# Kernel tuning notes

Hardware: AMD Instinct MI355X
Metric: run time of the kernel (lower is better)

Reference implementation:

```python
import jax, jax.numpy as jnp
import numpy as np


def setup_inputs() -> dict:
    key = jax.random.key(0)
    k1, k2, k3, k4 = jax.random.split(key, 4)
    B, T, C, D = 4, 2048, 1024, 128
    x = jax.random.normal(k1, (B, T, C), dtype=jnp.float32)
    # torch nn.Linear(in, out, bias=False) computes x @ W.T with W [out,in];
    # we store W as [in,out] so projection is x @ W (same math, transposed layout).
    Wq = jax.random.normal(k2, (C, D), dtype=jnp.float32) * (C ** -0.5)
    Wk = jax.random.normal(k3, (C, D), dtype=jnp.float32) * (C ** -0.5)
    Wv = jax.random.normal(k4, (C, D), dtype=jnp.float32) * (C ** -0.5)
    return {"x": x, "Wq": Wq, "Wk": Wk, "Wv": Wv}


def reference(x, Wq, Wk, Wv):
    B, T, C = x.shape
    D = Wq.shape[1]
    q = jnp.einsum("btc,cd->btd", x, Wq)
    k = jnp.einsum("btc,cd->btd", x, Wk)
    v = jnp.einsum("btc,cd->btd", x, Wv)
    scores = jnp.einsum("btd,bsd->bts", q, k) * (D ** -0.5)  # [B,T,T]
    causal = jnp.tril(jnp.ones((T, T), dtype=bool))
    scores = jnp.where(causal, scores, -jnp.inf)
    attn = jax.nn.softmax(scores, axis=-1)  # dropout_rate=0.0 -> identity
    return jnp.einsum("bts,bsd->btd", attn, v)
```

## Files before the change

kernel.cpp:

```cpp
#include <hip/hip_runtime.h>
#include <hip/hip_bf16.h>

typedef __attribute__((ext_vector_type(8))) short bf16x8;
typedef __attribute__((ext_vector_type(4))) short bf16x4;
typedef __attribute__((ext_vector_type(4))) float f32x4;

#define Tq 2048
#define Cq 1024
#define Dq 128

typedef const __attribute__((address_space(1))) void* gas_t;
typedef __attribute__((address_space(3))) void* las_t;

__device__ __forceinline__ short f2bf(float f) {
  unsigned u = __float_as_uint(f);
  u += 0x7fffu + ((u >> 16) & 1u);
  return (short)(u >> 16);
}

__global__ __launch_bounds__(256) void pack_w_kernel(const float* __restrict__ Wq_,
                                                     const float* __restrict__ Wk_,
                                                     const float* __restrict__ Wv_,
                                                     short* __restrict__ wt) {
  int tid = blockIdx.x * 256 + threadIdx.x;
  int y   = tid >> 14;
  int idx = tid & 16383;
  int kg  = idx >> 7;
  int n   = idx & 127;
  const float* W = (y == 0) ? Wq_ : (y == 1 ? Wk_ : Wv_);
  float scale = (y == 0) ? 0.08838834764831845f : 1.0f;
  bf16x8 o;
  #pragma unroll
  for (int j = 0; j < 8; ++j) o[j] = f2bf(W[(size_t)(kg * 8 + j) * Dq + n] * scale);
  *reinterpret_cast<bf16x8*>(wt + (size_t)y * 131072 + (size_t)n * 1024 + kg * 8) = o;
}

__global__ __launch_bounds__(128) void qkv_gemm_kernel(const float* __restrict__ x,
                                                       const short* __restrict__ wt,
                                                       short* __restrict__ qb,
                                                       short* __restrict__ kb2,
                                                       short* __restrict__ vt) {
  __shared__ float As[2][32][64];
  __shared__ short Bs[2][128][64];
  int y  = blockIdx.y;
  int bm = blockIdx.x;
  int w  = threadIdx.x >> 6, l = threadIdx.x & 63;
  int r  = l & 15, h = l >> 4;
  const short* wy = wt + (size_t)y * 131072;

  auto stage = [&](int t, int bi) {
    int k0 = t * 64;
    #pragma unroll
    for (int i = 0; i < 4; ++i) {
      int ia  = w * 4 + i;
      int row = ia * 4 + (l >> 4);
      int g   = l & 15;
      int sg  = (g & 8) | ((g & 7) ^ (row & 7));
      __builtin_amdgcn_global_load_lds(
          (gas_t)(x + (size_t)(bm * 32 + row) * Cq + k0 + sg * 4),
          (las_t)(&As[bi][ia * 4][0]), 16, 0, 0);
    }
    #pragma unroll
    for (int i = 0; i < 8; ++i) {
      int ib  = w * 8 + i;
      int row = ib * 8 + (l >> 3);
      int sc  = ((l & 7) ^ (row & 7)) * 8;
      __builtin_amdgcn_global_load_lds(
          (gas_t)(wy + (size_t)row * Cq + k0 + sc),
          (las_t)(&Bs[bi][ib * 8][0]), 16, 0, 0);
    }
  };

  f32x4 acc[2][4] = {};
  stage(0, 0);
  int cur = 0;
  for (int t = 0; t < 16; ++t, cur ^= 1) {
    stage(t + 1 < 16 ? t + 1 : t, cur ^ 1);
    asm volatile("s_waitcnt vmcnt(12)" ::: "memory");
    __builtin_amdgcn_s_barrier();
    __builtin_amdgcn_sched_barrier(0);
    bf16x8 af[2][2], bf[4][2];
    #pragma unroll
    for (int mi = 0; mi < 2; ++mi)
      #pragma unroll
      for (int kt = 0; kt < 2; ++kt) {
        int row = mi * 16 + r;
        int g0  = kt * 8 + h * 2;
        int s0  = (g0 & 8) | ((g0 & 7) ^ (row & 7));
        int g1  = g0 + 1;
        int s1  = (g1 & 8) | ((g1 & 7) ^ (row & 7));
        f32x4 fa = *reinterpret_cast<const f32x4*>(&As[cur][row][s0 * 4]);
        f32x4 fb = *reinterpret_cast<const f32x4*>(&As[cur][row][s1 * 4]);
        union { bf16x8 v; unsigned u[4]; } cv;
        asm("v_cvt_pk_bf16_f32 %0, %1, %2" : "=v"(cv.u[0]) : "v"(fa[0]), "v"(fa[1]));
        asm("v_cvt_pk_bf16_f32 %0, %1, %2" : "=v"(cv.u[1]) : "v"(fa[2]), "v"(fa[3]));
        asm("v_cvt_pk_bf16_f32 %0, %1, %2" : "=v"(cv.u[2]) : "v"(fb[0]), "v"(fb[1]));
        asm("v_cvt_pk_bf16_f32 %0, %1, %2" : "=v"(cv.u[3]) : "v"(fb[2]), "v"(fb[3]));
        af[mi][kt] = cv.v;
      }
    #pragma unroll
    for (int ni = 0; ni < 4; ++ni)
      #pragma unroll
      for (int kt = 0; kt < 2; ++kt) {
        int row = w * 64 + ni * 16 + r;
        bf[ni][kt] = *reinterpret_cast<const bf16x8*>(
            &Bs[cur][row][(kt * 32 + h * 8) ^ ((row & 7) << 3)]);
      }
    #pragma unroll
    for (int kt = 0; kt < 2; ++kt)
      #pragma unroll
      for (int mi = 0; mi < 2; ++mi)
        #pragma unroll
        for (int ni = 0; ni < 4; ++ni)
          acc[mi][ni] = __builtin_amdgcn_mfma_f32_16x16x32_bf16(af[mi][kt], bf[ni][kt], acc[mi][ni], 0, 0, 0);
    __builtin_amdgcn_sched_barrier(0);
    __builtin_amdgcn_s_barrier();
  }

  #pragma unroll
  for (int mi = 0; mi < 2; ++mi) {
    #pragma unroll
    for (int ni = 0; ni < 4; ++ni) {
      #pragma unroll
      for (int reg = 0; reg < 4; ++reg) {
        int m = bm * 32 + mi * 16 + h * 4 + reg;
        int n = w * 64 + ni * 16 + r;
        short s = f2bf(acc[mi][ni][reg]);
        if (y == 0)      qb[(size_t)m * Dq + n] = s;
        else if (y == 1) kb2[(size_t)m * Dq + n] = s;
        else {
          int bb = m >> 11, t2 = m & 2047;
          vt[((size_t)bb * Dq + n) * Tq + t2] = s;
        }
      }
    }
  }
}

__global__ __launch_bounds__(256, 4) void attn_kernel(const short* __restrict__ qb,
                                                      const short* __restrict__ kb2,
                                                      const short* __restrict__ vtb,
                                                      float* __restrict__ pacc,
                                                      float* __restrict__ pml) {
  __shared__ struct {
    short kb[2][32][128];
    short vb[2][128][32];
    short pb[4][16][40];
  } sm;

  int bid = blockIdx.x;
  int qi  = 31 - (bid >> 5);
  int b   = (bid >> 3) & 3;
  int c   = bid & 7;
  int tid = threadIdx.x;
  int w   = tid >> 6, l = tid & 63;
  int r   = l & 15, h = l >> 4;

  int qw = qi * 64 + w * 16;
  const short* kbB = kb2 + (size_t)b * Tq * Dq;
  const short* vtB = vtb + (size_t)b * Dq * Tq;

  bf16x8 aq[4];
  size_t qbase = ((size_t)b * Tq + qw + r) * Dq;
  #pragma unroll
  for (int kt = 0; kt < 4; ++kt)
    aq[kt] = *reinterpret_cast<const bf16x8*>(qb + qbase + kt * 32 + h * 8);

  int ntall = 2 * qi + 2;
  int clen  = (ntall + 7) >> 3;
  int tbeg  = c * clen;
  int tend  = ntall < tbeg + clen ? ntall : tbeg + clen;

  f32x4 acc[8] = {};
  float mrun = -1e30f, lrun = 0.0f;

  if (tbeg < tend) {
    auto stage = [&](int it, int bi) {
      int kv0 = it * 32;
      #pragma unroll
      for (int i2 = 0; i2 < 2; ++i2) {
        int i = w * 2 + i2;
        int row = i * 4 + (l >> 4);
        int sc  = ((l & 15) * 8) ^ ((row & 7) << 3);
        __builtin_amdgcn_global_load_lds(
            (gas_t)(kbB + (size_t)(kv0 + row) * Dq + sc),
            (las_t)(&sm.kb[bi][i * 4][0]), 16, 0, 0);
      }
      #pragma unroll
      for (int i2 = 0; i2 < 2; ++i2) {
        int i = w * 2 + i2;
        int row = i * 16 + (l >> 2);
        int sc  = ((l & 3) * 8) ^ ((row & 3) << 3);
        __builtin_amdgcn_global_load_lds(
            (gas_t)(vtB + (size_t)row * Tq + kv0 + sc),
            (las_t)(&sm.vb[bi][i * 16][0]), 16, 0, 0);
      }
    };

    stage(tbeg, 0);
    int cur = 0;
    for (int t = tbeg; t < tend; ++t, cur ^= 1) {
      stage(t + 1 < tend ? t + 1 : t, cur ^ 1);
      asm volatile("s_waitcnt vmcnt(4)" ::: "memory");
      __builtin_amdgcn_s_barrier();
      __builtin_amdgcn_sched_barrier(0);

      int kv0 = t * 32;
      bf16x8 kf[8];
      #pragma unroll
      for (int nt = 0; nt < 2; ++nt)
        #pragma unroll
        for (int kt = 0; kt < 4; ++kt) {
          int row = nt * 16 + r;
          kf[nt * 4 + kt] = *reinterpret_cast<const bf16x8*>(
              &sm.kb[cur][row][(kt * 32 + h * 8) ^ ((row & 7) << 3)]);
        }
      f32x4 s[2] = {};
      #pragma unroll
      for (int nt = 0; nt < 2; ++nt)
        #pragma unroll
        for (int kt = 0; kt < 4; ++kt)
          s[nt] = __builtin_amdgcn_mfma_f32_16x16x32_bf16(
              kf[nt * 4 + kt], aq[kt], s[nt], 0, 0, 0);

      bf16x8 vf[8];
      #pragma unroll
      for (int dt = 0; dt < 8; ++dt) {
        int row = dt * 16 + r;
        vf[dt] = *reinterpret_cast<const bf16x8*>(
            &sm.vb[cur][row][(h * 8) ^ ((row & 3) << 3)]);
      }

      if (kv0 + 31 > qw) {
        #pragma unroll
        for (int nt = 0; nt < 2; ++nt)
          #pragma unroll
          for (int reg = 0; reg < 4; ++reg)
            if (kv0 + nt * 16 + h * 4 + reg > qw + r) s[nt][reg] = -1e30f;
      }

      float mx = fmaxf(fmaxf(fmaxf(s[0][0], s[0][1]), fmaxf(s[0][2], s[0][3])),
                       fmaxf(fmaxf(s[1][0], s[1][1]), fmaxf(s[1][2], s[1][3])));
      mx = fmaxf(mx, __shfl_xor(mx, 16));
      mx = fmaxf(mx, __shfl_xor(mx, 32));
      float mnew  = fmaxf(mrun, mx);
      float alpha = __expf(mrun - mnew);
      mrun = mnew;
      float p[2][4];
      #pragma unroll
      for (int nt = 0; nt < 2; ++nt)
        #pragma unroll
        for (int reg = 0; reg < 4; ++reg)
          p[nt][reg] = s[nt][reg] > -1e29f ? __expf(s[nt][reg] - mnew) : 0.0f;
      float rsum = ((p[0][0] + p[0][1]) + (p[0][2] + p[0][3])) +
                   ((p[1][0] + p[1][1]) + (p[1][2] + p[1][3]));
      rsum += __shfl_xor(rsum, 16);
      rsum += __shfl_xor(rsum, 32);
      lrun = lrun * alpha + rsum;

      float af[4];
      #pragma unroll
      for (int reg = 0; reg < 4; ++reg) af[reg] = __shfl(alpha, h * 4 + reg);
      #pragma unroll
      for (int dt = 0; dt < 8; ++dt)
        #pragma unroll
        for (int reg = 0; reg < 4; ++reg) acc[dt][reg] *= af[reg];

      #pragma unroll
      for (int nt = 0; nt < 2; ++nt) {
        bf16x4 w4;
        #pragma unroll
        for (int reg = 0; reg < 4; ++reg) w4[reg] = f2bf(p[nt][reg]);
        *reinterpret_cast<bf16x4*>(&sm.pb[w][r][nt * 16 + h * 4]) = w4;
      }
      asm volatile("s_waitcnt lgkmcnt(0)" ::: "memory");
      __builtin_amdgcn_sched_barrier(0);
      bf16x8 ap = *reinterpret_cast<const bf16x8*>(&sm.pb[w][r][h * 8]);

      #pragma unroll
      for (int dt = 0; dt < 8; ++dt)
        acc[dt] = __builtin_amdgcn_mfma_f32_16x16x32_bf16(ap, vf[dt], acc[dt], 0, 0, 0);

      __builtin_amdgcn_sched_barrier(0);
      __builtin_amdgcn_s_barrier();
    }
  }

  if (h == 0) {
    pml[((size_t)bid * 64 + w * 16 + r) * 2 + 0] = mrun;
    pml[((size_t)bid * 64 + w * 16 + r) * 2 + 1] = lrun;
  }
  #pragma unroll
  for (int dt = 0; dt < 8; ++dt)
    #pragma unroll
    for (int reg = 0; reg < 4; ++reg) {
      int row = w * 16 + h * 4 + reg;
      pacc[((size_t)bid * 64 + row) * 128 + dt * 16 + r] = acc[dt][reg];
    }
}

__global__ __launch_bounds__(256) void combine_kernel(const float* __restrict__ pacc,
                                                      const float* __restrict__ pml,
                                                      float* __restrict__ out) {
  int gid = blockIdx.x * 256 + threadIdx.x;
  int rg  = gid >> 5;
  int c4  = (gid & 31) * 4;
  int task = rg >> 6;
  int row  = rg & 63;
  int qi = 31 - (task >> 2);
  int b  = task & 3;
  int bbase = task * 8;
  float M[8], L[8];
  float Ms = -1e30f;
  #pragma unroll
  for (int cc = 0; cc < 8; ++cc) {
    M[cc] = pml[((size_t)(bbase + cc) * 64 + row) * 2 + 0];
    L[cc] = pml[((size_t)(bbase + cc) * 64 + row) * 2 + 1];
    Ms = fmaxf(Ms, M[cc]);
  }
  float den = 0.0f;
  f32x4 num = {};
  #pragma unroll
  for (int cc = 0; cc < 8; ++cc) {
    float e = __expf(M[cc] - Ms);
    den += e * L[cc];
    f32x4 a = *reinterpret_cast<const f32x4*>(
        pacc + ((size_t)(bbase + cc) * 64 + row) * 128 + c4);
    num += a * e;
  }
  f32x4 o = num * (1.0f / den);
  *reinterpret_cast<f32x4*>(out + ((size_t)b * Tq + qi * 64 + row) * Dq + c4) = o;
}

extern "C" void kernel_launch(void* const* d_in, const int* in_sizes, int n_in,
                              void* d_out, int out_size, void* d_ws, size_t ws_size,
                              hipStream_t stream) {
  const float* x   = (const float*)d_in[0];
  const float* Wq_ = (const float*)d_in[1];
  const float* Wk_ = (const float*)d_in[2];
  const float* Wv_ = (const float*)d_in[3];
  float* out = (float*)d_out;
  char* ws = (char*)d_ws;
  short* wt   = (short*)(ws);
  short* qb   = (short*)(ws + 786432);
  short* kb   = (short*)(ws + 2883584);
  short* vt   = (short*)(ws + 4980736);
  float* pml  = (float*)(ws + 7077888);
  float* pacc = (float*)(ws + 7602176);

  hipLaunchKernelGGL(pack_w_kernel, dim3(192), dim3(256), 0, stream, Wq_, Wk_, Wv_, wt);
  hipLaunchKernelGGL(qkv_gemm_kernel, dim3(256, 3), dim3(128), 0, stream, x, wt, qb, kb, vt);
  hipLaunchKernelGGL(attn_kernel, dim3(1024), dim3(256), 0, stream, qb, kb, vt, pacc, pml);
  hipLaunchKernelGGL(combine_kernel, dim3(1024), dim3(256), 0, stream, pacc, pml, out);
}
```

Baseline: 56.63 us.

## Split causal attention into fixed-size KV chunks with variable chunk count per query tile

Replaces the fixed 8-way split of each query tile's KV range with fixed chunks of 4 KV tiles, so the number of blocks per query tile grows with its causal length (272 blocks per batch, 1088 total). This evens out per-block work and removes empty blocks from short query tiles. The combine kernel now reads a variable number of partials per row through closed-form offsets, and the workspace layout is shifted to hold the larger partial buffers. The costs are a serial loop to decode block indices, more partial results to write and merge, and fewer KV tiles per block, so each block does less pipelined work to hide its latency.

```diff
diff --git a/kernel.cpp b/kernel.cpp
--- a/kernel.cpp
+++ b/kernel.cpp
@@ -149,9 +149,11 @@
   } sm;
 
   int bid = blockIdx.x;
-  int qi  = 31 - (bid >> 5);
-  int b   = (bid >> 3) & 3;
-  int c   = bid & 7;
+  int b   = bid / 272;
+  int s0i = bid - b * 272;
+  int qi  = 31, off = 0;
+  while (s0i >= off + ((qi >> 1) + 1)) { off += (qi >> 1) + 1; --qi; }
+  int c   = s0i - off;
   int tid = threadIdx.x;
   int w   = tid >> 6, l = tid & 63;
   int r   = l & 15, h = l >> 4;
@@ -167,14 +169,13 @@
     aq[kt] = *reinterpret_cast<const bf16x8*>(qb + qbase + kt * 32 + h * 8);
 
   int ntall = 2 * qi + 2;
-  int clen  = (ntall + 7) >> 3;
-  int tbeg  = c * clen;
-  int tend  = ntall < tbeg + clen ? ntall : tbeg + clen;
+  int tbeg  = c * 4;
+  int tend  = ntall < tbeg + 4 ? ntall : tbeg + 4;
 
   f32x4 acc[8] = {};
   float mrun = -1e30f, lrun = 0.0f;
 
-  if (tbeg < tend) {
+  {
     auto stage = [&](int it, int bi) {
       int kv0 = it * 32;
       #pragma unroll
@@ -305,27 +306,27 @@
   int gid = blockIdx.x * 256 + threadIdx.x;
   int rg  = gid >> 5;
   int c4  = (gid & 31) * 4;
-  int task = rg >> 6;
-  int row  = rg & 63;
-  int qi = 31 - (task >> 2);
-  int b  = task & 3;
-  int bbase = task * 8;
-  float M[8], L[8];
+  int b      = rg >> 11;
+  int rowInB = rg & 2047;
+  int qi     = rowInB >> 6;
+  int row    = rowInB & 63;
+  int m    = qi >> 1;
+  int F    = (qi & 1) ? (m + 1) * (m + 2) : (m + 1) * (m + 1);
+  int base = b * 272 + 272 - F;
+  int nch  = m + 1;
+
   float Ms = -1e30f;
-  #pragma unroll
-  for (int cc = 0; cc < 8; ++cc) {
-    M[cc] = pml[((size_t)(bbase + cc) * 64 + row) * 2 + 0];
-    L[cc] = pml[((size_t)(bbase + cc) * 64 + row) * 2 + 1];
-    Ms = fmaxf(Ms, M[cc]);
-  }
+  for (int cc = 0; cc < nch; ++cc)
+    Ms = fmaxf(Ms, pml[((size_t)(base + cc) * 64 + row) * 2 + 0]);
   float den = 0.0f;
   f32x4 num = {};
-  #pragma unroll
-  for (int cc = 0; cc < 8; ++cc) {
-    float e = __expf(M[cc] - Ms);
-    den += e * L[cc];
+  for (int cc = 0; cc < nch; ++cc) {
+    float M = pml[((size_t)(base + cc) * 64 + row) * 2 + 0];
+    float L = pml[((size_t)(base + cc) * 64 + row) * 2 + 1];
+    float e = __expf(M - Ms);
+    den += e * L;
     f32x4 a = *reinterpret_cast<const f32x4*>(
-        pacc + ((size_t)(bbase + cc) * 64 + row) * 128 + c4);
+        pacc + ((size_t)(base + cc) * 64 + row) * 128 + c4);
     num += a * e;
   }
   f32x4 o = num * (1.0f / den);
@@ -346,10 +347,10 @@
   short* kb   = (short*)(ws + 2883584);
   short* vt   = (short*)(ws + 4980736);
   float* pml  = (float*)(ws + 7077888);
-  float* pacc = (float*)(ws + 7602176);
+  float* pacc = (float*)(ws + 7634944);
 
   hipLaunchKernelGGL(pack_w_kernel, dim3(192), dim3(256), 0, stream, Wq_, Wk_, Wv_, wt);
   hipLaunchKernelGGL(qkv_gemm_kernel, dim3(256, 3), dim3(128), 0, stream, x, wt, qb, kb, vt);
-  hipLaunchKernelGGL(attn_kernel, dim3(1024), dim3(256), 0, stream, qb, kb, vt, pacc, pml);
+  hipLaunchKernelGGL(attn_kernel, dim3(1088), dim3(256), 0, stream, qb, kb, vt, pacc, pml);
   hipLaunchKernelGGL(combine_kernel, dim3(1024), dim3(256), 0, stream, pacc, pml, out);
 }
```

Result: slower. 61.35 us (+8.3%).

## Keep P in registers via bpermute and store split-K partials as bf16

Applied to the files above, without the earlier changes.

Drops the LDS round-trip for the softmax probabilities. P is now packed to bf16 with v_cvt_pk_bf16_f32 and redistributed across lanes with ds_bpermute, and the PV MFMA operands are swapped so alpha rescaling needs no per-register shuffle. Partial accumulators written to the workspace and read by the combine kernel are now bf16 instead of fp32, which halves that traffic. The changes add extra rounding error in the partials and rely on the lane mapping of the bpermute-based transpose being correct.

```diff
diff --git a/kernel.cpp b/kernel.cpp
--- a/kernel.cpp
+++ b/kernel.cpp
@@ -16,6 +16,9 @@
   unsigned u = __float_as_uint(f);
   u += 0x7fffu + ((u >> 16) & 1u);
   return (short)(u >> 16);
+}
+__device__ __forceinline__ float bf2f(short s) {
+  return __uint_as_float(((unsigned)(unsigned short)s) << 16);
 }
 
 __global__ __launch_bounds__(256) void pack_w_kernel(const float* __restrict__ Wq_,
@@ -140,12 +143,11 @@
 __global__ __launch_bounds__(256, 4) void attn_kernel(const short* __restrict__ qb,
                                                       const short* __restrict__ kb2,
                                                       const short* __restrict__ vtb,
-                                                      float* __restrict__ pacc,
+                                                      short* __restrict__ pacc,
                                                       float* __restrict__ pml) {
   __shared__ struct {
     short kb[2][32][128];
     short vb[2][128][32];
-    short pb[4][16][40];
   } sm;
 
   int bid = blockIdx.x;
@@ -215,6 +217,7 @@
           kf[nt * 4 + kt] = *reinterpret_cast<const bf16x8*>(
               &sm.kb[cur][row][(kt * 32 + h * 8) ^ ((row & 7) << 3)]);
         }
+      __builtin_amdgcn_sched_barrier(0);
       f32x4 s[2] = {};
       #pragma unroll
       for (int nt = 0; nt < 2; ++nt)
@@ -251,35 +254,42 @@
       for (int nt = 0; nt < 2; ++nt)
         #pragma unroll
         for (int reg = 0; reg < 4; ++reg)
-          p[nt][reg] = s[nt][reg] > -1e29f ? __expf(s[nt][reg] - mnew) : 0.0f;
+          p[nt][reg] = s[nt][reg] > -1e29f ? __expf(s[nt][reg] - mrun) : 0.0f;
       float rsum = ((p[0][0] + p[0][1]) + (p[0][2] + p[0][3])) +
                    ((p[1][0] + p[1][1]) + (p[1][2] + p[1][3]));
       rsum += __shfl_xor(rsum, 16);
       rsum += __shfl_xor(rsum, 32);
       lrun = lrun * alpha + rsum;
-
-      float af[4];
-      #pragma unroll
-      for (int reg = 0; reg < 4; ++reg) af[reg] = __shfl(alpha, h * 4 + reg);
       #pragma unroll
       for (int dt = 0; dt < 8; ++dt)
         #pragma unroll
-        for (int reg = 0; reg < 4; ++reg) acc[dt][reg] *= af[reg];
-
-      #pragma unroll
-      for (int nt = 0; nt < 2; ++nt) {
-        bf16x4 w4;
-        #pragma unroll
-        for (int reg = 0; reg < 4; ++reg) w4[reg] = f2bf(p[nt][reg]);
-        *reinterpret_cast<bf16x4*>(&sm.pb[w][r][nt * 16 + h * 4]) = w4;
-      }
-      asm volatile("s_waitcnt lgkmcnt(0)" ::: "memory");
-      __builtin_amdgcn_sched_barrier(0);
-      bf16x8 ap = *reinterpret_cast<const bf16x8*>(&sm.pb[w][r][h * 8]);
+        for (int reg = 0; reg < 4; ++reg) acc[dt][reg] *= alpha;
+
+      unsigned wA0, wB0, wA1, wB1;
+      asm("v_cvt_pk_bf16_f32 %0, %1, %2" : "=v"(wA0) : "v"(p[0][0]), "v"(p[0][1]));
+      asm("v_cvt_pk_bf16_f32 %0, %1, %2" : "=v"(wB0) : "v"(p[0][2]), "v"(p[0][3]));
+      asm("v_cvt_pk_bf16_f32 %0, %1, %2" : "=v"(wA1) : "v"(p[1][0]), "v"(p[1][1]));
+      asm("v_cvt_pk_bf16_f32 %0, %1, %2" : "=v"(wB1) : "v"(p[1][2]), "v"(p[1][3]));
+      int a0 = (((h & 1) << 5) + r) << 2;
+      int a1 = a0 + 64;
+      unsigned yA0  = __builtin_amdgcn_ds_bpermute(a0, wA0);
+      unsigned yB0  = __builtin_amdgcn_ds_bpermute(a0, wB0);
+      unsigned yA0b = __builtin_amdgcn_ds_bpermute(a1, wA0);
+      unsigned yB0b = __builtin_amdgcn_ds_bpermute(a1, wB0);
+      unsigned yA1  = __builtin_amdgcn_ds_bpermute(a0, wA1);
+      unsigned yB1  = __builtin_amdgcn_ds_bpermute(a0, wB1);
+      unsigned yA1b = __builtin_amdgcn_ds_bpermute(a1, wA1);
+      unsigned yB1b = __builtin_amdgcn_ds_bpermute(a1, wB1);
+      bool hi = h >= 2;
+      union { unsigned u[4]; bf16x8 v; } pt;
+      pt.u[0] = hi ? yA1  : yA0;
+      pt.u[1] = hi ? yB1  : yB0;
+      pt.u[2] = hi ? yA1b : yA0b;
+      pt.u[3] = hi ? yB1b : yB0b;
 
       #pragma unroll
       for (int dt = 0; dt < 8; ++dt)
-        acc[dt] = __builtin_amdgcn_mfma_f32_16x16x32_bf16(ap, vf[dt], acc[dt], 0, 0, 0);
+        acc[dt] = __builtin_amdgcn_mfma_f32_16x16x32_bf16(vf[dt], pt.v, acc[dt], 0, 0, 0);
 
       __builtin_amdgcn_sched_barrier(0);
       __builtin_amdgcn_s_barrier();
@@ -290,16 +300,17 @@
     pml[((size_t)bid * 64 + w * 16 + r) * 2 + 0] = mrun;
     pml[((size_t)bid * 64 + w * 16 + r) * 2 + 1] = lrun;
   }
-  #pragma unroll
-  for (int dt = 0; dt < 8; ++dt)
-    #pragma unroll
-    for (int reg = 0; reg < 4; ++reg) {
-      int row = w * 16 + h * 4 + reg;
-      pacc[((size_t)bid * 64 + row) * 128 + dt * 16 + r] = acc[dt][reg];
-    }
-}
-
-__global__ __launch_bounds__(256) void combine_kernel(const float* __restrict__ pacc,
+  size_t prow = (size_t)bid * 64 + w * 16 + r;
+  #pragma unroll
+  for (int dt = 0; dt < 8; ++dt) {
+    bf16x4 o4;
+    #pragma unroll
+    for (int reg = 0; reg < 4; ++reg) o4[reg] = f2bf(acc[dt][reg]);
+    *reinterpret_cast<bf16x4*>(&pacc[prow * 128 + dt * 16 + h * 4]) = o4;
+  }
+}
+
+__global__ __launch_bounds__(256) void combine_kernel(const short* __restrict__ pacc,
                                                       const float* __restrict__ pml,
                                                       float* __restrict__ out) {
   int gid = blockIdx.x * 256 + threadIdx.x;
@@ -324,9 +335,10 @@
   for (int cc = 0; cc < 8; ++cc) {
     float e = __expf(M[cc] - Ms);
     den += e * L[cc];
-    f32x4 a = *reinterpret_cast<const f32x4*>(
+    bf16x4 a = *reinterpret_cast<const bf16x4*>(
         pacc + ((size_t)(bbase + cc) * 64 + row) * 128 + c4);
-    num += a * e;
+    #pragma unroll
+    for (int j = 0; j < 4; ++j) num[j] += bf2f(a[j]) * e;
   }
   f32x4 o = num * (1.0f / den);
   *reinterpret_cast<f32x4*>(out + ((size_t)b * Tq + qi * 64 + row) * Dq + c4) = o;
@@ -346,7 +358,7 @@
   short* kb   = (short*)(ws + 2883584);
   short* vt   = (short*)(ws + 4980736);
   float* pml  = (float*)(ws + 7077888);
-  float* pacc = (float*)(ws + 7602176);
+  short* pacc = (short*)(ws + 7602176);
 
   hipLaunchKernelGGL(pack_w_kernel, dim3(192), dim3(256), 0, stream, Wq_, Wk_, Wv_, wt);
   hipLaunchKernelGGL(qkv_gemm_kernel, dim3(256, 3), dim3(128), 0, stream, x, wt, qb, kb, vt);
```

After: 54.94 us. 1.03x faster.
